# Kernel optimization log

Hardware: AMD Instinct MI355X
Metric: run time of the kernel (lower is better)

The kernel has to match this reference:

```python
import jax, jax.numpy as jnp
import numpy as np

WS = 16          # window_size
NUM_HEADS = 6

def _rel_tables(ws):
    # SwinV2 continuous relative coords table, log-spaced, scaled by 8
    r = np.arange(-(ws - 1), ws, dtype=np.float32)
    t = np.stack(np.meshgrid(r, r, indexing='ij'), axis=-1)      # (2ws-1, 2ws-1, 2)
    t = t / (ws - 1) * 8.0
    t = np.sign(t) * np.log2(np.abs(t) + 1.0) / np.log2(8.0)
    c = np.stack(np.meshgrid(np.arange(ws), np.arange(ws), indexing='ij')).reshape(2, -1)
    rel = (c[:, :, None] - c[:, None, :]).transpose(1, 2, 0)     # (N, N, 2)
    rel[..., 0] += ws - 1
    rel[..., 1] += ws - 1
    rel[..., 0] *= 2 * ws - 1
    return jnp.asarray(t), jnp.asarray(rel.sum(-1))              # table, (N,N) int index

REL_TABLE, REL_INDEX = _rel_tables(WS)

def conv2d(x, w, b, pad=0, dil=1, groups=1):
    y = jax.lax.conv_general_dilated(
        x, w, (1, 1), [(pad, pad), (pad, pad)], rhs_dilation=(dil, dil),
        feature_group_count=groups, dimension_numbers=('NCHW', 'OIHW', 'NCHW'))
    return y + b[None, :, None, None]

def layernorm(x, g, b, eps=1e-5):
    mu = x.mean(-1, keepdims=True)
    var = ((x - mu) ** 2).mean(-1, keepdims=True)
    return (x - mu) * jax.lax.rsqrt(var + eps) * g + b

def _forward(x, p1_w, p1_b, pw_w, pw_b, dw_w, dw_b, dd_w, dd_b, p2_w, p2_b,
             ln_g, ln_b, qkv_w, q_bias, v_bias, logit_scale,
             cpb_w1, cpb_b1, cpb_w2, proj_w, proj_b):
    B, C, H, W = x.shape
    ws, nh = WS, NUM_HEADS
    N, hd = ws * ws, C // nh
    # ---- VAB: conv attention block ----
    y = jax.nn.gelu(conv2d(x, p1_w, p1_b), approximate=False)          # proj_1 + GELU
    a = conv2d(y, pw_w, pw_b)                                          # pointwise 1x1
    a = conv2d(a, dw_w, dw_b, pad=2, groups=C)                         # depthwise 5x5
    a = conv2d(a, dd_w, dd_b, pad=6, dil=3, groups=C)                  # depthwise 5x5 dil=3
    y = conv2d(y * a, p2_w, p2_b) + x                                  # proj_2 + residual
    y = jnp.transpose(y, (0, 2, 3, 1))                                 # B,H,W,C
    y = layernorm(y, ln_g, ln_b)                                       # pixel_norm
    # ---- window partition -> (B*nW, N, C) ----
    xw = y.reshape(B, H // ws, ws, W // ws, ws, C)
    xw = xw.transpose(0, 1, 3, 2, 4, 5).reshape(-1, N, C)
    # ---- SwinV2 cosine window attention ----
    qkv_b = jnp.concatenate([q_bias, jnp.zeros_like(v_bias), v_bias])
    qkv = (xw @ qkv_w.T + qkv_b).reshape(-1, N, 3, nh, hd).transpose(2, 0, 3, 1, 4)
    q, k, v = qkv[0], qkv[1], qkv[2]                                   # (B_, h, N, d)
    qn = q / jnp.maximum(jnp.linalg.norm(q, axis=-1, keepdims=True), 1e-12)
    kn = k / jnp.maximum(jnp.linalg.norm(k, axis=-1, keepdims=True), 1e-12)
    scale = jnp.exp(jnp.minimum(logit_scale, jnp.log(100.0)))          # clamp at 1/0.01
    attn = jnp.einsum('bhnd,bhmd->bhnm', qn, kn) * scale
    # CPB MLP bias: (2ws-1,2ws-1,2) -> heads, gathered by relative_position_index
    t = (jax.nn.relu(REL_TABLE @ cpb_w1.T + cpb_b1) @ cpb_w2.T).reshape(-1, nh)
    rpb = t[REL_INDEX.reshape(-1)].reshape(N, N, nh).transpose(2, 0, 1)
    attn = attn + 16.0 * jax.nn.sigmoid(rpb)
    attn = jax.nn.softmax(attn, axis=-1)
    out = jnp.einsum('bhnm,bhmd->bhnd', attn, v).transpose(0, 2, 1, 3).reshape(-1, N, C)
    out = out @ proj_w.T + proj_b
    # ---- window reverse -> NCHW ----
    out = out.reshape(B, H // ws, W // ws, ws, ws, C)
    out = out.transpose(0, 1, 3, 2, 4, 5).reshape(B, H, W, C)
    return jnp.transpose(out, (0, 3, 1, 2))

def setup_inputs():
    key = jax.random.key(0)
    ks = jax.random.split(key, 12)
    C, A = 192, 192
    rn = lambda k, shape, s=0.02: jax.random.normal(k, shape, jnp.float32) * s
    return {
        'x': jax.random.normal(ks[0], (4, C, 128, 128), jnp.float32),
        'p1_w': rn(ks[1], (A, C, 1, 1)), 'p1_b': jnp.zeros((A,), jnp.float32),
        'pw_w': rn(ks[2], (A, A, 1, 1)), 'pw_b': jnp.zeros((A,), jnp.float32),
        'dw_w': rn(ks[3], (A, 1, 5, 5), 0.05), 'dw_b': jnp.zeros((A,), jnp.float32),
        'dd_w': rn(ks[4], (A, 1, 5, 5), 0.05), 'dd_b': jnp.zeros((A,), jnp.float32),
        'p2_w': rn(ks[5], (C, A, 1, 1)), 'p2_b': jnp.zeros((C,), jnp.float32),
        'ln_g': jnp.ones((C,), jnp.float32), 'ln_b': jnp.zeros((C,), jnp.float32),
        'qkv_w': rn(ks[6], (3 * C, C)),
        'q_bias': jnp.zeros((C,), jnp.float32), 'v_bias': jnp.zeros((C,), jnp.float32),
        'logit_scale': jnp.log(10.0) * jnp.ones((NUM_HEADS, 1, 1), jnp.float32),
        'cpb_w1': rn(ks[7], (512, 2), 0.1), 'cpb_b1': jnp.zeros((512,), jnp.float32),
        'cpb_w2': rn(ks[8], (NUM_HEADS, 512), 0.1),
        'proj_w': rn(ks[9], (C, C)), 'proj_b': jnp.zeros((C,), jnp.float32),
    }

def reference(x, p1_w, p1_b, pw_w, pw_b, dw_w, dw_b, dd_w, dd_b, p2_w, p2_b,
              ln_g, ln_b, qkv_w, q_bias, v_bias, logit_scale,
              cpb_w1, cpb_b1, cpb_w2, proj_w, proj_b):
    return _forward(x, p1_w, p1_b, pw_w, pw_b, dw_w, dw_b, dd_w, dd_b, p2_w, p2_b,
                    ln_g, ln_b, qkv_w, q_bias, v_bias, logit_scale,
                    cpb_w1, cpb_b1, cpb_w2, proj_w, proj_b)
```

## Files before the change

kernel.cpp:

```cpp
#include <hip/hip_runtime.h>
#include <hip/hip_bf16.h>
#include <math.h>

#define HWC 16384
#define CCH 192
#define LDA 200

typedef __attribute__((ext_vector_type(8))) short short8x;
typedef __attribute__((ext_vector_type(4))) float f32x4;

__device__ __forceinline__ float b2f(unsigned int u){
  union { unsigned int i; float f; } x; x.i = (u & 0xffffu) << 16; return x.f;
}
__device__ __forceinline__ unsigned short f2b(float f){
  union { float f; unsigned int i; } x; x.f = f;
  unsigned int r = x.i + 0x7FFFu + ((x.i >> 16) & 1u);
  return (unsigned short)(r >> 16);
}
__device__ __forceinline__ float gelu_exact(float v){
  return 0.5f * v * (1.0f + erff(v * 0.70710678118654752440f));
}

__global__ __launch_bounds__(256) void cast_w_kernel(
    const float* __restrict__ qkvw, const float* __restrict__ projw,
    const float* __restrict__ p1w,  const float* __restrict__ pww,
    const float* __restrict__ p2w,  const float* __restrict__ dww,
    const float* __restrict__ ddw,
    unsigned short* __restrict__ wq,  unsigned short* __restrict__ wprj,
    unsigned short* __restrict__ wp1, unsigned short* __restrict__ wpa,
    unsigned short* __restrict__ wp2, float* __restrict__ dwt,
    float* __restrict__ ddt)
{
  int i = blockIdx.x*256 + threadIdx.x;
  if (i < 110592) wq[i] = f2b(qkvw[i]);
  if (i < 36864){
    wprj[i] = f2b(projw[i]);
    wp1[i]  = f2b(p1w[i]);
    wpa[i]  = f2b(pww[i]);
    wp2[i]  = f2b(p2w[i]);
  }
  if (i < 4800){
    int t = i / 192, c = i - t*192;
    dwt[i] = dww[c*25 + t];
    ddt[i] = ddw[c*25 + t];
  }
}

__global__ __launch_bounds__(256) void tx_kernel(
    const float* __restrict__ in, float* __restrict__ xt32,
    unsigned short* __restrict__ x16)
{
  __shared__ float xs[CCH*68];
  const int tid = threadIdx.x;
  const int pix0 = blockIdx.x * 64;
  const int bb = pix0 >> 14;
  const int hw0 = pix0 & (HWC-1);
  const long base = (long)bb * CCH * HWC + hw0;
  #pragma unroll 8
  for (int i=0;i<48;i++){
    int idx = tid + i*256;
    int ci = idx >> 6, pix = idx & 63;
    xs[ci*68 + pix] = in[base + (long)ci*HWC + pix];
  }
  __syncthreads();
  #pragma unroll 8
  for (int i=0;i<48;i++){
    int idx = tid + i*256;
    int pix = idx / 192, ci = idx - pix*192;
    float v = xs[ci*68 + pix];
    long g = (long)(pix0 + pix)*CCH + ci;
    xt32[g] = v;
    x16[g]  = f2b(v);
  }
}

template<int MODE>
__global__ __launch_bounds__(256, 3) void pw_mfma(
    const unsigned short* __restrict__ in0,
    const unsigned short* __restrict__ in1,
    const unsigned short* __restrict__ w16,
    const float* __restrict__ bias,
    const float* __restrict__ xres,
    const float* __restrict__ gam, const float* __restrict__ bet,
    unsigned short* __restrict__ out16)
{
  __shared__ unsigned short sA[128*LDA];
  __shared__ float reds[128*2], reds2[128*2];
  const int tid = threadIdx.x;
  const int m0 = blockIdx.x * 128;
  #pragma unroll
  for (int i=0;i<12;i++){
    int idx = tid + i*256;
    int row = idx / 24, oct = idx - row*24;
    long g = (long)(m0+row)*CCH + oct*8;
    uint4 vy = *(const uint4*)(in0 + g);
    if (MODE == 2){
      uint4 va = *(const uint4*)(in1 + g);
      unsigned int yy[4] = {vy.x, vy.y, vy.z, vy.w};
      unsigned int aa[4] = {va.x, va.y, va.z, va.w};
      unsigned int rr[4];
      #pragma unroll
      for (int wq2=0; wq2<4; wq2++){
        float lo = b2f(yy[wq2]) * b2f(aa[wq2]);
        float hi = b2f(yy[wq2] >> 16) * b2f(aa[wq2] >> 16);
        rr[wq2] = (unsigned int)f2b(lo) | ((unsigned int)f2b(hi) << 16);
      }
      uint4 vp; vp.x=rr[0]; vp.y=rr[1]; vp.z=rr[2]; vp.w=rr[3];
      *(uint4*)&sA[row*LDA + oct*8] = vp;
    } else {
      *(uint4*)&sA[row*LDA + oct*8] = vy;
    }
  }
  __syncthreads();
  const int wv = tid >> 6, lane = tid & 63;
  const int wm = (wv & 1) * 64;
  const int wn = (wv >> 1) * 96;
  const int l15 = lane & 15, q = lane >> 4;
  f32x4 acc[4][6];
  #pragma unroll
  for (int mi=0;mi<4;mi++)
    #pragma unroll
    for (int ni=0;ni<6;ni++) acc[mi][ni] = (f32x4){0.f,0.f,0.f,0.f};
  #pragma unroll
  for (int kk=0; kk<6; kk++){
    const int k0 = kk*32;
    short8x af[4], bf[6];
    #pragma unroll
    for (int mi=0; mi<4; mi++)
      af[mi] = *(const short8x*)&sA[(wm + mi*16 + l15)*LDA + k0 + q*8];
    #pragma unroll
    for (int ni=0; ni<6; ni++)
      bf[ni] = *(const short8x*)(w16 + (long)(wn + ni*16 + l15)*CCH + k0 + q*8);
    #pragma unroll
    for (int mi=0; mi<4; mi++)
      #pragma unroll
      for (int ni=0; ni<6; ni++)
        acc[mi][ni] = __builtin_amdgcn_mfma_f32_16x16x32_bf16(af[mi], bf[ni], acc[mi][ni], 0,0,0);
  }
  float bv[6];
  #pragma unroll
  for (int ni=0; ni<6; ni++) bv[ni] = bias[wn + ni*16 + l15];

  if (MODE != 2){
    #pragma unroll
    for (int mi=0; mi<4; mi++){
      #pragma unroll
      for (int r=0; r<4; r++){
        long gp = (long)(m0 + wm + mi*16 + q*4 + r)*CCH + wn;
        #pragma unroll
        for (int ni=0; ni<6; ni++){
          float v = acc[mi][ni][r] + bv[ni];
          if (MODE == 0) v = gelu_exact(v);
          out16[gp + ni*16 + l15] = f2b(v);
        }
      }
    }
  } else {
    const int slot = wv >> 1;
    #pragma unroll
    for (int mi=0; mi<4; mi++){
      #pragma unroll
      for (int r=0; r<4; r++){
        int pixl = wm + mi*16 + q*4 + r;
        long gp = (long)(m0 + pixl)*CCH + wn;
        float s = 0.f, s2 = 0.f;
        #pragma unroll
        for (int ni=0; ni<6; ni++){
          float v = acc[mi][ni][r] + bv[ni] + xres[gp + ni*16 + l15];
          acc[mi][ni][r] = v;
          s += v; s2 = fmaf(v, v, s2);
        }
        s  += __shfl_xor(s, 1);  s  += __shfl_xor(s, 2);
        s  += __shfl_xor(s, 4);  s  += __shfl_xor(s, 8);
        s2 += __shfl_xor(s2, 1); s2 += __shfl_xor(s2, 2);
        s2 += __shfl_xor(s2, 4); s2 += __shfl_xor(s2, 8);
        if (l15 == 0){ reds[pixl*2 + slot] = s; reds2[pixl*2 + slot] = s2; }
      }
    }
    __syncthreads();
    #pragma unroll
    for (int mi=0; mi<4; mi++){
      #pragma unroll
      for (int r=0; r<4; r++){
        int pixl = wm + mi*16 + q*4 + r;
        long gp = (long)(m0 + pixl)*CCH + wn;
        float st  = reds[pixl*2] + reds[pixl*2+1];
        float s2t = reds2[pixl*2] + reds2[pixl*2+1];
        float mu = st * (1.0f/192.0f);
        float var = s2t * (1.0f/192.0f) - mu*mu;
        float rs = rsqrtf(var + 1e-5f);
        #pragma unroll
        for (int ni=0; ni<6; ni++){
          int co = wn + ni*16 + l15;
          float z = (acc[mi][ni][r] - mu) * rs * gam[co] + bet[co];
          out16[gp + ni*16 + l15] = f2b(z);
        }
      }
    }
  }
}

template<int PAD, int DIL>
__global__ __launch_bounds__(256) void dw_nhwc(
    const unsigned short* __restrict__ in16, const float* __restrict__ wT,
    const float* __restrict__ bias, unsigned short* __restrict__ out16)
{
  const int g = blockIdx.x;
  const int wid = (g & 7) * 768 + (g >> 3);
  const int t = wid*256 + threadIdx.x;
  const int c8 = t % 24, pix = t / 24;
  const int row = (pix >> 7) & 127, col = pix & 127;
  const int c0 = c8 * 8;
  const long ibase = (long)(pix & ~(HWC-1)) * CCH;
  float acc[8];
  {
    float4 b0 = *(const float4*)&bias[c0], b1 = *(const float4*)&bias[c0+4];
    acc[0]=b0.x; acc[1]=b0.y; acc[2]=b0.z; acc[3]=b0.w;
    acc[4]=b1.x; acc[5]=b1.y; acc[6]=b1.z; acc[7]=b1.w;
  }
  #pragma unroll
  for (int kh=0; kh<5; kh++){
    int ih = row + kh*DIL - PAD;
    if ((unsigned)ih < 128u){
      #pragma unroll
      for (int kw=0; kw<5; kw++){
        int iw = col + kw*DIL - PAD;
        if ((unsigned)iw < 128u){
          uint4 v = *(const uint4*)(in16 + ibase + (long)(ih*128 + iw)*CCH + c0);
          const float* wp = wT + (kh*5 + kw)*CCH + c0;
          float4 w0 = *(const float4*)wp, w1 = *(const float4*)(wp + 4);
          unsigned int uu[4] = {v.x, v.y, v.z, v.w};
          float wa[8] = {w0.x, w0.y, w0.z, w0.w, w1.x, w1.y, w1.z, w1.w};
          #pragma unroll
          for (int j=0; j<8; j++){
            float xv = b2f(uu[j>>1] >> ((j&1)*16));
            acc[j] = fmaf(wa[j], xv, acc[j]);
          }
        }
      }
    }
  }
  unsigned int rr[4];
  #pragma unroll
  for (int wq2=0; wq2<4; wq2++)
    rr[wq2] = (unsigned int)f2b(acc[wq2*2]) | ((unsigned int)f2b(acc[wq2*2+1]) << 16);
  uint4 o; o.x=rr[0]; o.y=rr[1]; o.z=rr[2]; o.w=rr[3];
  *(uint4*)(out16 + (long)pix*CCH + c0) = o;
}

__global__ __launch_bounds__(256, 3) void qkv_mfma(
    const unsigned short* __restrict__ z16,
    const unsigned short* __restrict__ w16,
    const float* __restrict__ qb, const float* __restrict__ vb,
    float* __restrict__ qkv)
{
  __shared__ unsigned short sA[128*LDA];
  const int tid = threadIdx.x;
  const int m0 = blockIdx.x * 128;
  const int s  = blockIdx.y;
  #pragma unroll
  for (int i=0;i<12;i++){
    int idx = tid + i*256;
    int row = idx / 24, oct = idx - row*24;
    uint4 v = *(const uint4*)(z16 + (long)(m0+row)*CCH + oct*8);
    *(uint4*)&sA[row*LDA + oct*8] = v;
  }
  __syncthreads();
  const int wv = tid >> 6, lane = tid & 63;
  const int wm = (wv & 1) * 64;
  const int wn = (wv >> 1) * 96;
  const int l15 = lane & 15, q = lane >> 4;
  const unsigned short* wbase = w16 + (long)(s*192)*CCH;
  f32x4 acc[4][6];
  #pragma unroll
  for (int mi=0;mi<4;mi++)
    #pragma unroll
    for (int ni=0;ni<6;ni++) acc[mi][ni] = (f32x4){0.f,0.f,0.f,0.f};
  #pragma unroll
  for (int kk=0; kk<6; kk++){
    const int k0 = kk*32;
    short8x af[4], bf[6];
    #pragma unroll
    for (int mi=0; mi<4; mi++)
      af[mi] = *(const short8x*)&sA[(wm + mi*16 + l15)*LDA + k0 + q*8];
    #pragma unroll
    for (int ni=0; ni<6; ni++)
      bf[ni] = *(const short8x*)(wbase + (long)(wn + ni*16 + l15)*CCH + k0 + q*8);
    #pragma unroll
    for (int mi=0; mi<4; mi++)
      #pragma unroll
      for (int ni=0; ni<6; ni++)
        acc[mi][ni] = __builtin_amdgcn_mfma_f32_16x16x32_bf16(af[mi], bf[ni], acc[mi][ni], 0,0,0);
  }
  #pragma unroll
  for (int ni=0; ni<6; ni++){
    int co = wn + ni*16 + l15;
    float bv = (s==0) ? qb[co] : ((s==2) ? vb[co] : 0.0f);
    #pragma unroll
    for (int mi=0; mi<4; mi++){
      #pragma unroll
      for (int r=0; r<4; r++){
        int pix = m0 + wm + mi*16 + q*4 + r;
        qkv[(long)pix*576 + s*192 + co] = acc[mi][ni][r] + bv;
      }
    }
  }
}

__device__ __forceinline__ float cpb_coord(int a){
  float r = ((float)a - 15.0f) * (8.0f/15.0f);
  float t = log2f(fabsf(r) + 1.0f) * (1.0f/3.0f);
  return (r < 0.f) ? -t : t;
}
__global__ __launch_bounds__(128) void cpb_mlp_kernel(
    const float* __restrict__ w1, const float* __restrict__ b1,
    const float* __restrict__ w2, float* __restrict__ tbl6)
{
  int e = blockIdx.x;
  int a = e / 31, bb = e - a*31;
  float t0 = cpb_coord(a), t1 = cpb_coord(bb);
  float p[6] = {0,0,0,0,0,0};
  for (int hh = threadIdx.x; hh < 512; hh += 128){
    float hid = t0*w1[hh*2] + t1*w1[hh*2+1] + b1[hh];
    hid = fmaxf(hid, 0.0f);
    #pragma unroll
    for (int hd=0; hd<6; hd++) p[hd] = fmaf(hid, w2[hd*512 + hh], p[hd]);
  }
  __shared__ float red[6][128];
  #pragma unroll
  for (int hd=0; hd<6; hd++) red[hd][threadIdx.x] = p[hd];
  __syncthreads();
  if (threadIdx.x < 6){
    float sum = 0.f;
    for (int i=0;i<128;i++) sum += red[threadIdx.x][i];
    tbl6[e*6 + threadIdx.x] = sum;
  }
}
__global__ __launch_bounds__(256) void cpb_expand_kernel(
    const float* __restrict__ tbl6, float* __restrict__ bias)
{
  int idx = blockIdx.x*256 + threadIdx.x;
  int h = idx >> 16;
  int rem = idx & 65535;
  int i = rem >> 8, j = rem & 255;
  int dy = (i>>4) - (j>>4) + 15;
  int dx = (i&15) - (j&15) + 15;
  float v = tbl6[(dy*31+dx)*6 + h];
  bias[idx] = 16.0f / (1.0f + __expf(-v)) - 16.0f;
}

#define KSP 40
#define VTP 264
__global__ __launch_bounds__(256) void attn_mfma(
    const float* __restrict__ qkv, const float* __restrict__ bias,
    const float* __restrict__ ls, unsigned short* __restrict__ aout)
{
  __shared__ unsigned short ks[256*KSP];
  __shared__ unsigned short vt[32*VTP];
  __shared__ unsigned short ps[4][64*KSP];
  unsigned short* qs = &ps[0][0];

  const int win = blockIdx.x, h = blockIdx.y;
  const int t = threadIdx.x;
  const int bb = win >> 6;
  const int wy = (win >> 3) & 7, wx = win & 7;
  const float sc = __expf(fminf(ls[h], 4.60517018598809136804f));

  {
    const int ty = t >> 4, tx = t & 15;
    const int pix = bb*HWC + (wy*16+ty)*128 + wx*16 + tx;
    const float* row = qkv + (long)pix*576 + h*32;
    float qv[32], kv[32];
    float sq = 0.f, sk = 0.f;
    #pragma unroll
    for (int d=0; d<32; d+=4){
      float4 a = *(const float4*)(row + d);
      float4 b = *(const float4*)(row + 192 + d);
      qv[d]=a.x; qv[d+1]=a.y; qv[d+2]=a.z; qv[d+3]=a.w;
      kv[d]=b.x; kv[d+1]=b.y; kv[d+2]=b.z; kv[d+3]=b.w;
      sq += a.x*a.x + a.y*a.y + a.z*a.z + a.w*a.w;
      sk += b.x*b.x + b.y*b.y + b.z*b.z + b.w*b.w;
    }
    float qinv = sc / fmaxf(sqrtf(sq), 1e-12f);
    float kinv = 1.0f / fmaxf(sqrtf(sk), 1e-12f);
    union { unsigned short u[32]; uint4 v4[4]; } qp, kp;
    #pragma unroll
    for (int d=0; d<32; d++){ qp.u[d] = f2b(qv[d]*qinv); kp.u[d] = f2b(kv[d]*kinv); }
    #pragma unroll
    for (int o=0;o<4;o++){
      *(uint4*)&qs[t*KSP + o*8] = qp.v4[o];
      *(uint4*)&ks[t*KSP + o*8] = kp.v4[o];
    }
  }
  {
    const int d = t & 31, kt = t >> 5;
    union { unsigned short u[32]; uint4 v4[4]; } vp;
    #pragma unroll 4
    for (int i=0;i<32;i++){
      int key = kt*32 + i;
      int pixk = bb*HWC + (wy*16 + (key>>4))*128 + wx*16 + (key&15);
      vp.u[i] = f2b(qkv[(long)pixk*576 + 384 + h*32 + d]);
    }
    #pragma unroll
    for (int o=0;o<4;o++) *(uint4*)&vt[d*VTP + kt*32 + o*8] = vp.v4[o];
  }
  __syncthreads();

  const int wv = t >> 6, lane = t & 63;
  const int l15 = lane & 15, q = lane >> 4;
  short8x qa[4];
  #pragma unroll
  for (int mi=0; mi<4; mi++)
    qa[mi] = *(const short8x*)&qs[(wv*64 + mi*16 + l15)*KSP + q*8];
  __syncthreads();

  f32x4 oacc[4][2], lsum[4];
  #pragma unroll
  for (int mi=0;mi<4;mi++){
    oacc[mi][0] = (f32x4){0.f,0.f,0.f,0.f};
    oacc[mi][1] = (f32x4){0.f,0.f,0.f,0.f};
    lsum[mi]    = (f32x4){0.f,0.f,0.f,0.f};
  }
  const float* bias_h = bias + (h << 16);
  unsigned short* myps = ps[wv];

  for (int kt=0; kt<8; kt++){
    const int k0 = kt*32;
    short8x kb0 = *(const short8x*)&ks[(k0 + l15)*KSP + q*8];
    short8x kb1 = *(const short8x*)&ks[(k0 + 16 + l15)*KSP + q*8];
    f32x4 s[4][2];
    #pragma unroll
    for (int mi=0; mi<4; mi++){
      f32x4 z0 = (f32x4){0.f,0.f,0.f,0.f};
      s[mi][0] = __builtin_amdgcn_mfma_f32_16x16x32_bf16(qa[mi], kb0, z0, 0,0,0);
      s[mi][1] = __builtin_amdgcn_mfma_f32_16x16x32_bf16(qa[mi], kb1, z0, 0,0,0);
    }
    #pragma unroll
    for (int mi=0; mi<4; mi++){
      #pragma unroll
      for (int r=0; r<4; r++){
        int rowq = wv*64 + mi*16 + q*4 + r;
        const float* brow = bias_h + rowq*256 + k0;
        float e0 = __expf(fminf(s[mi][0][r] + brow[l15],      30.f));
        float e1 = __expf(fminf(s[mi][1][r] + brow[16 + l15], 30.f));
        lsum[mi][r] += e0 + e1;
        myps[(mi*16 + q*4 + r)*KSP + l15]      = f2b(e0);
        myps[(mi*16 + q*4 + r)*KSP + 16 + l15] = f2b(e1);
      }
    }
    short8x vb0 = *(const short8x*)&vt[(l15)*VTP      + k0 + q*8];
    short8x vb1 = *(const short8x*)&vt[(16 + l15)*VTP + k0 + q*8];
    #pragma unroll
    for (int mi=0; mi<4; mi++){
      short8x pa = *(const short8x*)&myps[(mi*16 + l15)*KSP + q*8];
      oacc[mi][0] = __builtin_amdgcn_mfma_f32_16x16x32_bf16(pa, vb0, oacc[mi][0], 0,0,0);
      oacc[mi][1] = __builtin_amdgcn_mfma_f32_16x16x32_bf16(pa, vb1, oacc[mi][1], 0,0,0);
    }
  }
  #pragma unroll
  for (int mi=0; mi<4; mi++){
    #pragma unroll
    for (int r=0; r<4; r++){
      float v = lsum[mi][r];
      v += __shfl_xor(v, 1);
      v += __shfl_xor(v, 2);
      v += __shfl_xor(v, 4);
      v += __shfl_xor(v, 8);
      lsum[mi][r] = v;
    }
  }
  #pragma unroll
  for (int mi=0; mi<4; mi++){
    #pragma unroll
    for (int r=0; r<4; r++){
      int rowq = wv*64 + mi*16 + q*4 + r;
      int pixo = bb*HWC + (wy*16 + (rowq>>4))*128 + wx*16 + (rowq&15);
      float inv = 1.0f / lsum[mi][r];
      aout[(long)pixo*CCH + h*32 + l15]      = f2b(oacc[mi][0][r]*inv);
      aout[(long)pixo*CCH + h*32 + 16 + l15] = f2b(oacc[mi][1][r]*inv);
    }
  }
}

__global__ __launch_bounds__(256, 3) void proj_mfma(
    const unsigned short* __restrict__ a16,
    const unsigned short* __restrict__ w16,
    const float* __restrict__ bias,
    float* __restrict__ outp)
{
  __shared__ unsigned short sB[128*LDA];
  const int tid = threadIdx.x;
  const int n0 = blockIdx.x * 128;
  #pragma unroll
  for (int i=0;i<12;i++){
    int idx = tid + i*256;
    int row = idx / 24, oct = idx - row*24;
    uint4 v = *(const uint4*)(a16 + (long)(n0+row)*CCH + oct*8);
    *(uint4*)&sB[row*LDA + oct*8] = v;
  }
  __syncthreads();
  const int wv = tid >> 6, lane = tid & 63;
  const int wm = (wv & 1) * 96;
  const int wn = (wv >> 1) * 64;
  const int l15 = lane & 15, q = lane >> 4;
  f32x4 acc[6][4];
  #pragma unroll
  for (int mi=0;mi<6;mi++)
    #pragma unroll
    for (int ni=0;ni<4;ni++) acc[mi][ni] = (f32x4){0.f,0.f,0.f,0.f};
  #pragma unroll
  for (int kk=0; kk<6; kk++){
    const int k0 = kk*32;
    short8x af[6], bf[4];
    #pragma unroll
    for (int mi=0; mi<6; mi++)
      af[mi] = *(const short8x*)(w16 + (long)(wm + mi*16 + l15)*CCH + k0 + q*8);
    #pragma unroll
    for (int ni=0; ni<4; ni++)
      bf[ni] = *(const short8x*)&sB[(wn + ni*16 + l15)*LDA + k0 + q*8];
    #pragma unroll
    for (int mi=0; mi<6; mi++)
      #pragma unroll
      for (int ni=0; ni<4; ni++)
        acc[mi][ni] = __builtin_amdgcn_mfma_f32_16x16x32_bf16(af[mi], bf[ni], acc[mi][ni], 0,0,0);
  }
  #pragma unroll
  for (int mi=0; mi<6; mi++){
    #pragma unroll
    for (int r=0; r<4; r++){
      int co = wm + mi*16 + q*4 + r;
      float bv = bias[co];
      #pragma unroll
      for (int ni=0; ni<4; ni++){
        int pix = n0 + wn + ni*16 + l15;
        int b = pix >> 14, hw = pix & (HWC-1);
        outp[((long)b*CCH + co)*HWC + hw] = acc[mi][ni][r] + bv;
      }
    }
  }
}

extern "C" void kernel_launch(void* const* d_in, const int* in_sizes, int n_in,
                              void* d_out, int out_size, void* d_ws, size_t ws_size,
                              hipStream_t stream)
{
  const float* x       = (const float*)d_in[0];
  const float* p1_w    = (const float*)d_in[1];
  const float* p1_b    = (const float*)d_in[2];
  const float* pw_w    = (const float*)d_in[3];
  const float* pw_b    = (const float*)d_in[4];
  const float* dw_w    = (const float*)d_in[5];
  const float* dw_b    = (const float*)d_in[6];
  const float* dd_w    = (const float*)d_in[7];
  const float* dd_b    = (const float*)d_in[8];
  const float* p2_w    = (const float*)d_in[9];
  const float* p2_b    = (const float*)d_in[10];
  const float* ln_g    = (const float*)d_in[11];
  const float* ln_b    = (const float*)d_in[12];
  const float* qkv_w   = (const float*)d_in[13];
  const float* q_bias  = (const float*)d_in[14];
  const float* v_bias  = (const float*)d_in[15];
  const float* lscale  = (const float*)d_in[16];
  const float* cpb_w1  = (const float*)d_in[17];
  const float* cpb_b1  = (const float*)d_in[18];
  const float* cpb_w2  = (const float*)d_in[19];
  const float* proj_w  = (const float*)d_in[20];
  const float* proj_b  = (const float*)d_in[21];

  float* ws = (float*)d_ws;
  const long A = 12582912L;
  unsigned short* X16  = (unsigned short*)ws;
  unsigned short* Y16  = (unsigned short*)(ws + A/2);
  unsigned short* A16  = (unsigned short*)(ws + A);
  unsigned short* T16  = (unsigned short*)(ws + A + A/2);
  float* XT32 = ws + 2*A;
  float* R0   = ws;
  unsigned short* Z16  = (unsigned short*)(ws + 3*A);
  unsigned short* AO16 = Z16;
  float* DWT = ws + 3*A + A/2;
  float* DDT = DWT + 4800;
  unsigned short* WQ   = (unsigned short*)(DDT + 4800);
  unsigned short* WPRJ = WQ + 110592;
  unsigned short* WP1  = WPRJ + 36864;
  unsigned short* WPA  = WP1 + 36864;
  unsigned short* WP2  = WPA + 36864;
  float* RB = ws + 4*A;
  float* T6 = RB + 393216;

  cast_w_kernel<<<432, 256, 0, stream>>>(qkv_w, proj_w, p1_w, pw_w, p2_w, dw_w, dd_w,
                                         WQ, WPRJ, WP1, WPA, WP2, DWT, DDT);
  cpb_mlp_kernel<<<961, 128, 0, stream>>>(cpb_w1, cpb_b1, cpb_w2, T6);
  cpb_expand_kernel<<<1536, 256, 0, stream>>>(T6, RB);

  tx_kernel<<<1024, 256, 0, stream>>>(x, XT32, X16);

  pw_mfma<0><<<512, 256, 0, stream>>>(X16, nullptr, WP1, p1_b, nullptr, nullptr, nullptr, Y16);
  pw_mfma<1><<<512, 256, 0, stream>>>(Y16, nullptr, WPA, pw_b, nullptr, nullptr, nullptr, A16);
  dw_nhwc<2,1><<<6144, 256, 0, stream>>>(A16, DWT, dw_b, T16);
  dw_nhwc<6,3><<<6144, 256, 0, stream>>>(T16, DDT, dd_b, A16);
  pw_mfma<2><<<512, 256, 0, stream>>>(Y16, A16, WP2, p2_b, XT32, ln_g, ln_b, Z16);

  qkv_mfma<<<dim3(512, 3), 256, 0, stream>>>(Z16, WQ, q_bias, v_bias, R0);

  attn_mfma<<<dim3(256, 6), 256, 0, stream>>>(R0, RB, lscale, AO16);

  proj_mfma<<<512, 256, 0, stream>>>(AO16, WPRJ, proj_b, (float*)d_out);
}
```

Baseline: 512.8 us.

## Fuse q/k normalization and bf16 window layout into QKV GEMM epilogue

```diff
diff --git a/kernel.cpp b/kernel.cpp
--- a/kernel.cpp
+++ b/kernel.cpp
@@ -248,11 +248,12 @@
   *(uint4*)(out16 + (long)pix*CCH + c0) = o;
 }
 
-__global__ __launch_bounds__(256, 3) void qkv_mfma(
+__global__ __launch_bounds__(256, 3) void qkv_fused(
     const unsigned short* __restrict__ z16,
     const unsigned short* __restrict__ w16,
     const float* __restrict__ qb, const float* __restrict__ vb,
-    float* __restrict__ qkv)
+    const float* __restrict__ ls,
+    unsigned short* __restrict__ qkvb)
 {
   __shared__ unsigned short sA[128*LDA];
   const int tid = threadIdx.x;
@@ -292,17 +293,50 @@
       for (int ni=0; ni<6; ni++)
         acc[mi][ni] = __builtin_amdgcn_mfma_f32_16x16x32_bf16(af[mi], bf[ni], acc[mi][ni], 0,0,0);
   }
-  #pragma unroll
-  for (int ni=0; ni<6; ni++){
+  float bvv[6];
+  #pragma unroll
+  for (int ni=0;ni<6;ni++){
     int co = wn + ni*16 + l15;
-    float bv = (s==0) ? qb[co] : ((s==2) ? vb[co] : 0.0f);
-    #pragma unroll
-    for (int mi=0; mi<4; mi++){
-      #pragma unroll
-      for (int r=0; r<4; r++){
-        int pix = m0 + wm + mi*16 + q*4 + r;
-        qkv[(long)pix*576 + s*192 + co] = acc[mi][ni][r] + bv;
-      }
+    bvv[ni] = (s==0) ? qb[co] : ((s==2) ? vb[co] : 0.0f);
+  }
+  float sc_[3] = {1.f, 1.f, 1.f};
+  if (s == 0){
+    #pragma unroll
+    for (int hp=0;hp<3;hp++)
+      sc_[hp] = __expf(fminf(ls[(wn>>5)+hp], 4.60517018598809136804f));
+  }
+  unsigned short* dst = qkvb + (long)s * 12582912;
+  const int head0 = wn >> 5;
+  #pragma unroll
+  for (int mi=0; mi<4; mi++){
+    #pragma unroll
+    for (int r=0; r<4; r++){
+      int pix = m0 + wm + mi*16 + q*4 + r;
+      int hw = pix & (HWC-1);
+      int win = (pix>>14)*64 + ((hw>>11)&7)*8 + ((hw>>4)&7);
+      int tok = ((hw>>7)&15)*16 + (hw&15);
+      long ob = (long)win*49152 + (long)tok*32;
+      float vv[6];
+      #pragma unroll
+      for (int ni=0;ni<6;ni++) vv[ni] = acc[mi][ni][r] + bvv[ni];
+      if (s != 2){
+        float s0 = vv[0]*vv[0] + vv[1]*vv[1];
+        float s1 = vv[2]*vv[2] + vv[3]*vv[3];
+        float s2 = vv[4]*vv[4] + vv[5]*vv[5];
+        #pragma unroll
+        for (int xm=1; xm<16; xm<<=1){
+          s0 += __shfl_xor(s0, xm);
+          s1 += __shfl_xor(s1, xm);
+          s2 += __shfl_xor(s2, xm);
+        }
+        float i0 = sc_[0]/fmaxf(sqrtf(s0),1e-12f);
+        float i1 = sc_[1]/fmaxf(sqrtf(s1),1e-12f);
+        float i2 = sc_[2]/fmaxf(sqrtf(s2),1e-12f);
+        vv[0]*=i0; vv[1]*=i0; vv[2]*=i1; vv[3]*=i1; vv[4]*=i2; vv[5]*=i2;
+      }
+      #pragma unroll
+      for (int ni=0;ni<6;ni++)
+        dst[ob + (long)(head0 + (ni>>1))*8192 + (ni&1)*16 + l15] = f2b(vv[ni]);
     }
   }
 }
@@ -352,66 +386,42 @@
 #define KSP 40
 #define VTP 264
 __global__ __launch_bounds__(256) void attn_mfma(
-    const float* __restrict__ qkv, const float* __restrict__ bias,
-    const float* __restrict__ ls, unsigned short* __restrict__ aout)
+    const unsigned short* __restrict__ qkvb, const float* __restrict__ bias,
+    unsigned short* __restrict__ aout)
 {
   __shared__ unsigned short ks[256*KSP];
   __shared__ unsigned short vt[32*VTP];
   __shared__ unsigned short ps[4][64*KSP];
-  unsigned short* qs = &ps[0][0];
-
   const int win = blockIdx.x, h = blockIdx.y;
   const int t = threadIdx.x;
-  const int bb = win >> 6;
-  const int wy = (win >> 3) & 7, wx = win & 7;
-  const float sc = __expf(fminf(ls[h], 4.60517018598809136804f));
+  const long base = ((long)(win*6 + h)) << 13;
+  const unsigned short* Qg = qkvb + base;
+  const unsigned short* Kg = Qg + 12582912;
+  const unsigned short* Vg = Kg + 12582912;
 
   {
-    const int ty = t >> 4, tx = t & 15;
-    const int pix = bb*HWC + (wy*16+ty)*128 + wx*16 + tx;
-    const float* row = qkv + (long)pix*576 + h*32;
-    float qv[32], kv[32];
-    float sq = 0.f, sk = 0.f;
-    #pragma unroll
-    for (int d=0; d<32; d+=4){
-      float4 a = *(const float4*)(row + d);
-      float4 b = *(const float4*)(row + 192 + d);
-      qv[d]=a.x; qv[d+1]=a.y; qv[d+2]=a.z; qv[d+3]=a.w;
-      kv[d]=b.x; kv[d+1]=b.y; kv[d+2]=b.z; kv[d+3]=b.w;
-      sq += a.x*a.x + a.y*a.y + a.z*a.z + a.w*a.w;
-      sk += b.x*b.x + b.y*b.y + b.z*b.z + b.w*b.w;
-    }
-    float qinv = sc / fmaxf(sqrtf(sq), 1e-12f);
-    float kinv = 1.0f / fmaxf(sqrtf(sk), 1e-12f);
-    union { unsigned short u[32]; uint4 v4[4]; } qp, kp;
-    #pragma unroll
-    for (int d=0; d<32; d++){ qp.u[d] = f2b(qv[d]*qinv); kp.u[d] = f2b(kv[d]*kinv); }
-    #pragma unroll
-    for (int o=0;o<4;o++){
-      *(uint4*)&qs[t*KSP + o*8] = qp.v4[o];
-      *(uint4*)&ks[t*KSP + o*8] = kp.v4[o];
-    }
-  }
-  {
-    const int d = t & 31, kt = t >> 5;
+    const unsigned short* kr = Kg + t*32;
+    uint4 k0v = *(const uint4*)(kr+0);
+    uint4 k1v = *(const uint4*)(kr+8);
+    uint4 k2v = *(const uint4*)(kr+16);
+    uint4 k3v = *(const uint4*)(kr+24);
+    *(uint4*)&ks[t*KSP +  0] = k0v;
+    *(uint4*)&ks[t*KSP +  8] = k1v;
+    *(uint4*)&ks[t*KSP + 16] = k2v;
+    *(uint4*)&ks[t*KSP + 24] = k3v;
     union { unsigned short u[32]; uint4 v4[4]; } vp;
-    #pragma unroll 4
-    for (int i=0;i<32;i++){
-      int key = kt*32 + i;
-      int pixk = bb*HWC + (wy*16 + (key>>4))*128 + wx*16 + (key&15);
-      vp.u[i] = f2b(qkv[(long)pixk*576 + 384 + h*32 + d]);
-    }
-    #pragma unroll
-    for (int o=0;o<4;o++) *(uint4*)&vt[d*VTP + kt*32 + o*8] = vp.v4[o];
-  }
-  __syncthreads();
-
+    const unsigned short* vr = Vg + t*32;
+    #pragma unroll
+    for (int o=0;o<4;o++) vp.v4[o] = *(const uint4*)(vr + o*8);
+    #pragma unroll
+    for (int d=0; d<32; d++) vt[d*VTP + t] = vp.u[d];
+  }
   const int wv = t >> 6, lane = t & 63;
   const int l15 = lane & 15, q = lane >> 4;
   short8x qa[4];
   #pragma unroll
   for (int mi=0; mi<4; mi++)
-    qa[mi] = *(const short8x*)&qs[(wv*64 + mi*16 + l15)*KSP + q*8];
+    qa[mi] = *(const short8x*)(Qg + (wv*64 + mi*16 + l15)*32 + q*8);
   __syncthreads();
 
   f32x4 oacc[4][2], lsum[4];
@@ -429,12 +439,14 @@
     short8x kb0 = *(const short8x*)&ks[(k0 + l15)*KSP + q*8];
     short8x kb1 = *(const short8x*)&ks[(k0 + 16 + l15)*KSP + q*8];
     f32x4 s[4][2];
+    __builtin_amdgcn_s_setprio(1);
     #pragma unroll
     for (int mi=0; mi<4; mi++){
       f32x4 z0 = (f32x4){0.f,0.f,0.f,0.f};
       s[mi][0] = __builtin_amdgcn_mfma_f32_16x16x32_bf16(qa[mi], kb0, z0, 0,0,0);
       s[mi][1] = __builtin_amdgcn_mfma_f32_16x16x32_bf16(qa[mi], kb1, z0, 0,0,0);
     }
+    __builtin_amdgcn_s_setprio(0);
     #pragma unroll
     for (int mi=0; mi<4; mi++){
       #pragma unroll
@@ -450,12 +462,14 @@
     }
     short8x vb0 = *(const short8x*)&vt[(l15)*VTP      + k0 + q*8];
     short8x vb1 = *(const short8x*)&vt[(16 + l15)*VTP + k0 + q*8];
+    __builtin_amdgcn_s_setprio(1);
     #pragma unroll
     for (int mi=0; mi<4; mi++){
       short8x pa = *(const short8x*)&myps[(mi*16 + l15)*KSP + q*8];
       oacc[mi][0] = __builtin_amdgcn_mfma_f32_16x16x32_bf16(pa, vb0, oacc[mi][0], 0,0,0);
       oacc[mi][1] = __builtin_amdgcn_mfma_f32_16x16x32_bf16(pa, vb1, oacc[mi][1], 0,0,0);
     }
+    __builtin_amdgcn_s_setprio(0);
   }
   #pragma unroll
   for (int mi=0; mi<4; mi++){
@@ -469,6 +483,7 @@
       lsum[mi][r] = v;
     }
   }
+  const int bb = win >> 6, wy = (win >> 3) & 7, wx = win & 7;
   #pragma unroll
   for (int mi=0; mi<4; mi++){
     #pragma unroll
@@ -574,7 +589,7 @@
   unsigned short* A16  = (unsigned short*)(ws + A);
   unsigned short* T16  = (unsigned short*)(ws + A + A/2);
   float* XT32 = ws + 2*A;
-  float* R0   = ws;
+  unsigned short* QKVB = (unsigned short*)ws;
   unsigned short* Z16  = (unsigned short*)(ws + 3*A);
   unsigned short* AO16 = Z16;
   float* DWT = ws + 3*A + A/2;
@@ -600,9 +615,9 @@
   dw_nhwc<6,3><<<6144, 256, 0, stream>>>(T16, DDT, dd_b, A16);
   pw_mfma<2><<<512, 256, 0, stream>>>(Y16, A16, WP2, p2_b, XT32, ln_g, ln_b, Z16);
 
-  qkv_mfma<<<dim3(512, 3), 256, 0, stream>>>(Z16, WQ, q_bias, v_bias, R0);
-
-  attn_mfma<<<dim3(256, 6), 256, 0, stream>>>(R0, RB, lscale, AO16);
+  qkv_fused<<<dim3(512, 3), 256, 0, stream>>>(Z16, WQ, q_bias, v_bias, lscale, QKVB);
+
+  attn_mfma<<<dim3(256, 6), 256, 0, stream>>>(QKVB, RB, AO16);
 
   proj_mfma<<<512, 256, 0, stream>>>(AO16, WPRJ, proj_b, (float*)d_out);
 }
```

New measurement: 503.9 us. No clear change (-1.7%).
